# Kernel tuning notes

Hardware: AMD Instinct MI355X
Metric: run time of the kernel (lower is better)

Reference implementation:

```python
import jax, jax.numpy as jnp
import numpy as np

N_NODES = 100000
N_EDGES = 1600000
IN_CH = 128
TYPE_EMB = 32
OUT_CH = 128
N_REL = 8
N_BASES = 8
N_NTYPES = 8
FEAT = IN_CH + TYPE_EMB  # 160, RGCNConv input dim after concat


def setup_inputs() -> dict:
    key = jax.random.key(0)
    ks = jax.random.split(key, 9)
    x = jax.random.normal(ks[0], (N_NODES, IN_CH), dtype=jnp.float32)
    node_type_ids = jax.random.randint(ks[1], (N_NODES,), 0, N_NTYPES)
    edge_index = jax.random.randint(ks[2], (2, N_EDGES), 0, N_NODES)
    edge_type = jax.random.randint(ks[3], (N_EDGES,), 0, N_REL)
    emb_table = jax.random.normal(ks[4], (N_NTYPES, TYPE_EMB), dtype=jnp.float32)
    bases = jax.random.normal(ks[5], (N_BASES, FEAT, OUT_CH), dtype=jnp.float32) * (1.0 / np.sqrt(FEAT))
    comp = jax.random.normal(ks[6], (N_REL, N_BASES), dtype=jnp.float32) * (1.0 / np.sqrt(N_BASES))
    root_w = jax.random.normal(ks[7], (FEAT, OUT_CH), dtype=jnp.float32) * (1.0 / np.sqrt(FEAT))
    bias = jnp.zeros((OUT_CH,), dtype=jnp.float32)
    return {"x": x, "node_type_ids": node_type_ids, "edge_index": edge_index,
            "edge_type": edge_type, "emb_table": emb_table, "bases": bases,
            "comp": comp, "root_w": root_w, "bias": bias}


def reference(x, node_type_ids, edge_index, edge_type, emb_table, bases, comp, root_w, bias):
    N = x.shape[0]
    # node-type embedding lookup + concat
    h = jnp.concatenate([x, emb_table[node_type_ids]], axis=1)  # [N, FEAT]
    # basis decomposition: per-relation weights [R, FEAT, OUT]
    weight = jnp.einsum('rb,bio->rio', comp, bases)
    src, dst = edge_index[0], edge_index[1]
    h_src = h[src]  # [E, FEAT] -- dominant gather
    # root/self transform + bias
    out = h @ root_w + bias
    # PyG RGCNConv default aggr='mean': per-relation mean over incoming edges, summed across relations
    for r in range(weight.shape[0]):
        m = (edge_type == r).astype(h.dtype)  # [E]
        s = jax.ops.segment_sum(h_src * m[:, None], dst, num_segments=N)  # [N, FEAT]
        c = jax.ops.segment_sum(m, dst, num_segments=N)                    # [N]
        mean_r = s / jnp.maximum(c, 1.0)[:, None]
        out = out + mean_r @ weight[r]
    # dropout is identity in eval mode
    return jax.nn.relu(out)
```

## Files before the change

kernel.cpp:

```cpp
#include <hip/hip_runtime.h>

#define NN 100000
#define NE 1600000
#define INC 128
#define TE 32
#define OC 128
#define NR 8
#define NBASES 8
#define FT 160
#define KP 168
#define KW 160
#define TN 32
#define NBKT 3125
#define NCH 128
#define EPB 12500
#define CAP 896

typedef float f32x4 __attribute__((ext_vector_type(4)));
typedef float f32x2 __attribute__((ext_vector_type(2)));
typedef __bf16 bf16x8 __attribute__((ext_vector_type(8)));

__device__ __forceinline__ unsigned f2bf1(float f) {
    unsigned u = __float_as_uint(f);
    return (u + 0x7fffu + ((u >> 16) & 1u)) >> 16;
}

__device__ __forceinline__ float bflo(unsigned u) { return __uint_as_float(u << 16); }
__device__ __forceinline__ float bfhi(unsigned u) { return __uint_as_float(u & 0xFFFF0000u); }

__device__ __forceinline__ unsigned cvtpk(float a, float b) {
    unsigned r;
    asm("v_cvt_pk_bf16_f32 %0, %1, %2" : "=v"(r) : "v"(a), "v"(b));
    return r;
}

__device__ __forceinline__ int bscan_excl(int v, int* tmp) {
    int tid = threadIdx.x;
    tmp[tid] = v; __syncthreads();
#pragma unroll
    for (int d = 1; d < 256; d <<= 1) {
        int t = (tid >= d) ? tmp[tid - d] : 0;
        __syncthreads();
        tmp[tid] += t;
        __syncthreads();
    }
    return tmp[tid] - v;
}

__global__ __launch_bounds__(256) void k_prep(
    const float* __restrict__ x, const int* __restrict__ nt,
    const float* __restrict__ emb, const float* __restrict__ comp,
    const float* __restrict__ bases, const float* __restrict__ rootw,
    const int* __restrict__ ei,
    unsigned short* __restrict__ h, unsigned short* __restrict__ Wt,
    int* __restrict__ ghist, int* __restrict__ total) {
    __shared__ int hist[NBKT];
    int tid = threadIdx.x;
    int b = blockIdx.x;
    if (b < NCH) {
        for (int j = tid; j < NBKT; j += 256) hist[j] = 0;
        __syncthreads();
        int e0 = b * EPB;
#pragma unroll
        for (int k = 0; k < 49; k++) {
            int i = k * 256 + tid;
            if (i < EPB) atomicAdd(&hist[ei[NE + e0 + i] >> 5], 1);
        }
        __syncthreads();
        int* g = ghist + (size_t)b * NBKT;
        for (int j = tid; j < NBKT; j += 256) {
            int v = hist[j];
            g[j] = v;
            if (v) atomicAdd(&total[j], v);
        }
        return;
    }
    int idx = (b - NCH) * 256 + tid;
    if (idx < 9 * 128 * KW) {
        int ridx = idx / (128 * KW);
        int rem  = idx % (128 * KW);
        int o = rem / KW;
        int k = rem % KW;
        float v;
        if (ridx < NR) {
            v = 0.f;
#pragma unroll
            for (int bb = 0; bb < NBASES; bb++)
                v += comp[ridx * NBASES + bb] * bases[(bb * FT + k) * OC + o];
        } else {
            v = rootw[k * OC + o];
        }
        Wt[idx] = (unsigned short)f2bf1(v);
    }
    if (idx < NN * 16) {
        int n = idx / 16, c = idx % 16;
        const float* p = x + (size_t)n * INC + c * 8;
        f32x4 v0 = *(const f32x4*)p, v1 = *(const f32x4*)(p + 4);
        uint4 o;
        o.x = f2bf1(v0.x) | (f2bf1(v0.y) << 16);
        o.y = f2bf1(v0.z) | (f2bf1(v0.w) << 16);
        o.z = f2bf1(v1.x) | (f2bf1(v1.y) << 16);
        o.w = f2bf1(v1.z) | (f2bf1(v1.w) << 16);
        *(uint4*)(h + (size_t)n * INC + c * 8) = o;
    }
}

__global__ __launch_bounds__(256) void k_scanoff(const int* __restrict__ total,
                                                 int* __restrict__ ghist,
                                                 int* __restrict__ bstart) {
    __shared__ int tot[NBKT];
    __shared__ int tmp[256];
    int tid = threadIdx.x;
    for (int j = tid; j < NBKT; j += 256) tot[j] = total[j];
    __syncthreads();
    int i0 = tid * 13, s = 0;
    int loc[13];
#pragma unroll
    for (int i = 0; i < 13; i++) {
        int j = i0 + i;
        loc[i] = (j < NBKT) ? tot[j] : 0;
        s += loc[i];
    }
    int run = bscan_excl(s, tmp);
#pragma unroll
    for (int i = 0; i < 13; i++) {
        int j = i0 + i;
        if (j < NBKT) tot[j] = run;
        run += loc[i];
    }
    __syncthreads();
    if (blockIdx.x == 0) {
        for (int j = tid; j < NBKT; j += 256) bstart[j] = tot[j];
        if (tid == 0) bstart[NBKT] = NE;
    }
    int j = blockIdx.x * 256 + tid;
    if (j < NBKT) {
        int run2 = tot[j];
#pragma unroll 4
        for (int b = 0; b < NCH; b++) {
            int v = ghist[(size_t)b * NBKT + j];
            ghist[(size_t)b * NBKT + j] = run2;
            run2 += v;
        }
    }
}

__global__ __launch_bounds__(256) void k_scatter(const int* __restrict__ ei, const int* __restrict__ et,
                                                 const int* __restrict__ nt,
                                                 const int* __restrict__ ghist, unsigned* __restrict__ slots) {
    __shared__ int cur[NBKT];
    int tid = threadIdx.x, b = blockIdx.x;
    for (int j = tid; j < NBKT; j += 256) cur[j] = ghist[(size_t)b * NBKT + j];
    __syncthreads();
    int e0 = b * EPB;
#pragma unroll
    for (int kk = 0; kk < 52; kk += 4) {
        int sv[4], dv[4], rv[4], tv[4];
#pragma unroll
        for (int u = 0; u < 4; u++) {
            int i = (kk + u) * 256 + tid;
            int e = e0 + ((i < EPB) ? i : 0);
            sv[u] = ei[e]; dv[u] = ei[NE + e]; rv[u] = et[e];
            if (i >= EPB) dv[u] = -1;
        }
#pragma unroll
        for (int u = 0; u < 4; u++) tv[u] = nt[sv[u]];
#pragma unroll
        for (int u = 0; u < 4; u++) {
            if (dv[u] >= 0) {
                int pos = atomicAdd(&cur[dv[u] >> 5], 1);
                slots[pos] = (unsigned)sv[u] | ((unsigned)rv[u] << 17)
                           | ((unsigned)(dv[u] & 31) << 20) | ((unsigned)tv[u] << 25);
            }
        }
    }
}

__global__ __launch_bounds__(256, 6) void k_mega(
    const unsigned short* __restrict__ h, const int* __restrict__ nt,
    const float* __restrict__ emb, const float* __restrict__ bias,
    const unsigned short* __restrict__ Wt, const int* __restrict__ bstart,
    const unsigned* __restrict__ slots, float* __restrict__ out) {
    __shared__ unsigned short featmem[2][TN * KP];
    __shared__ unsigned sl[CAP];
    __shared__ unsigned pkl[256];
    __shared__ float embf[256];

    const int tid = threadIdx.x;
    const int lane = tid & 63;
    const int wave = tid >> 6;
    const int j = blockIdx.x;
    const int n0 = j * TN;

    unsigned* sl_in = reinterpret_cast<unsigned*>(&featmem[0][0]);
    int* hist = reinterpret_cast<int*>(&featmem[0][0]) + CAP;
    int* tmp  = reinterpret_cast<int*>(&featmem[0][0]) + CAP + 256;

    int s0 = bstart[j];
    int m = bstart[j + 1] - s0; if (m > CAP) m = CAP;
    for (int i = tid; i < m; i += 256) sl_in[i] = slots[s0 + i];
    hist[tid] = 0;
    __syncthreads();
    for (int i = tid; i < m; i += 256) {
        unsigned v = sl_in[i];
        atomicAdd(&hist[((v >> 17) & 7u) * 32u + ((v >> 20) & 31u)], 1);
    }
    __syncthreads();
    int v0 = hist[tid];
    int ex = bscan_excl(v0, tmp);
    pkl[tid] = (unsigned)ex | ((unsigned)v0 << 16);
    hist[tid] = ex;
    __syncthreads();
    for (int i = tid; i < m; i += 256) {
        unsigned v = sl_in[i];
        int p = atomicAdd(&hist[((v >> 17) & 7u) * 32u + ((v >> 20) & 31u)], 1);
        sl[p] = (v & 0x1FFFFu) | (((v >> 25) & 7u) << 17);
    }
    __syncthreads();

    if (tid < 256) embf[tid] = emb[tid];
    for (int i = tid; i < TN * 20; i += 256) {
        int nl = i / 20, c = i % 20, n = n0 + nl;
        uint4 v;
        if (c < 16) {
            v = *reinterpret_cast<const uint4*>(h + (size_t)n * INC + c * 8);
        } else {
            int t = nt[n];
            const float* p = emb + t * TE + (c - 16) * 8;
            f32x4 a = *(const f32x4*)p, bq = *(const f32x4*)(p + 4);
            v.x = f2bf1(a.x) | (f2bf1(a.y) << 16);
            v.y = f2bf1(a.z) | (f2bf1(a.w) << 16);
            v.z = f2bf1(bq.x) | (f2bf1(bq.y) << 16);
            v.w = f2bf1(bq.z) | (f2bf1(bq.w) << 16);
        }
        *reinterpret_cast<uint4*>(&featmem[0][nl * KP + c * 8]) = v;
    }

    f32x4 acc[4];
#pragma unroll
    for (int t = 0; t < 4; t++) acc[t] = (f32x4){0.f, 0.f, 0.f, 0.f};

    auto mfma_pass = [&](int ridx, const unsigned short* fm) {
        const unsigned short* fA = fm + (lane & 15) * KP + ((lane >> 4) * 8);
        const unsigned short* gB = Wt + (size_t)ridx * 128 * KW
                                   + (wave * 32 + (lane & 15)) * KW + ((lane >> 4) * 8);
#pragma unroll
        for (int kc = 0; kc < 5; kc++) {
            bf16x8 a0 = *reinterpret_cast<const bf16x8*>(fA + 0 * 16 * KP + kc * 32);
            bf16x8 a1 = *reinterpret_cast<const bf16x8*>(fA + 1 * 16 * KP + kc * 32);
#pragma unroll
            for (int ct = 0; ct < 2; ct++) {
                bf16x8 b = *reinterpret_cast<const bf16x8*>(gB + ct * 16 * KW + kc * 32);
                acc[0 * 2 + ct] = __builtin_amdgcn_mfma_f32_16x16x32_bf16(a0, b, acc[0 * 2 + ct], 0, 0, 0);
                acc[1 * 2 + ct] = __builtin_amdgcn_mfma_f32_16x16x32_bf16(a1, b, acc[1 * 2 + ct], 0, 0, 0);
            }
        }
    };

    const int g = tid >> 4, l = tid & 15;
    const unsigned* hw = reinterpret_cast<const unsigned*>(h);

    auto agg_pass = [&](int r, unsigned short* fm) {
        int b0 = r * 32 + 2 * g;
        unsigned pk0 = pkl[b0], pk1 = pkl[b0 + 1];
        int sbeg = (int)(pk0 & 0xffffu);
        int e1 = (int)(pk1 & 0xffffu);
        int send = e1 + (int)(pk1 >> 16);
        f32x2 sa[5];
#pragma unroll
        for (int i = 0; i < 5; i++) sa[i] = (f32x2){0.f, 0.f};
        float run = 0.f;
        for (int e = sbeg; e < send; e += 4) {
            uint4 wv[4]; int tt[4];
#pragma unroll
            for (int u = 0; u < 4; u++) {
                int eu = e + u; if (eu >= send) eu = send - 1;
                unsigned v = sl[eu];
                wv[u] = *reinterpret_cast<const uint4*>(hw + (size_t)(v & 0x1FFFFu) * 64 + 4 * l);
                tt[u] = (int)((v >> 17) & 7u);
            }
#pragma unroll
            for (int u = 0; u < 4; u++) {
                if (e + u < send) {
                    sa[0] += (f32x2){bflo(wv[u].x), bfhi(wv[u].x)};
                    sa[1] += (f32x2){bflo(wv[u].y), bfhi(wv[u].y)};
                    sa[2] += (f32x2){bflo(wv[u].z), bfhi(wv[u].z)};
                    sa[3] += (f32x2){bflo(wv[u].w), bfhi(wv[u].w)};
                    sa[4] += *reinterpret_cast<const f32x2*>(&embf[tt[u] * 32 + 2 * l]);
                    run += 1.f;
                    int nx = e + u + 1;
                    if (nx == e1 || nx == send) {
                        int q = (e + u >= e1) ? 1 : 0;
                        float inv = __builtin_amdgcn_rcpf(run);
                        f32x2 m0 = sa[0] * inv, m1 = sa[1] * inv, m2 = sa[2] * inv,
                              m3 = sa[3] * inv, m4 = sa[4] * inv;
                        unsigned* fp = reinterpret_cast<unsigned*>(fm + (2 * g + q) * KP);
                        uint4 o;
                        o.x = cvtpk(m0.x, m0.y);
                        o.y = cvtpk(m1.x, m1.y);
                        o.z = cvtpk(m2.x, m2.y);
                        o.w = cvtpk(m3.x, m3.y);
                        *reinterpret_cast<uint4*>(fp + 4 * l) = o;
                        fp[64 + l] = cvtpk(m4.x, m4.y);
#pragma unroll
                        for (int i = 0; i < 5; i++) sa[i] = (f32x2){0.f, 0.f};
                        run = 0.f;
                    }
                }
            }
        }
#pragma unroll
        for (int q = 0; q < 2; q++) {
            if ((pkl[b0 + q] >> 16) == 0u) {
                unsigned* fp = reinterpret_cast<unsigned*>(fm + (2 * g + q) * KP);
                *reinterpret_cast<uint4*>(fp + 4 * l) = (uint4){0u, 0u, 0u, 0u};
                fp[64 + l] = 0u;
            }
        }
    };

    __syncthreads();
    int prev = 8;
    for (int r = 0; r < NR; r++) {
        agg_pass(r, &featmem[(r + 1) & 1][0]);
        mfma_pass(prev, &featmem[r & 1][0]);
        prev = r;
        __syncthreads();
    }
    mfma_pass(7, &featmem[0][0]);

    const int rq = lane >> 4;
#pragma unroll
    for (int ct = 0; ct < 2; ct++) {
        int col = wave * 32 + ct * 16 + (lane & 15);
        float bv = bias[col];
#pragma unroll
        for (int rt = 0; rt < 2; rt++) {
#pragma unroll
            for (int i = 0; i < 4; i++) {
                int n = n0 + rt * 16 + rq * 4 + i;
                float v = acc[rt * 2 + ct][i] + bv;
                out[(size_t)n * OC + col] = v > 0.f ? v : 0.f;
            }
        }
    }
}

extern "C" void kernel_launch(void* const* d_in, const int* in_sizes, int n_in,
                              void* d_out, int out_size, void* d_ws, size_t ws_size,
                              hipStream_t stream) {
    const float* x     = (const float*)d_in[0];
    const int*   ntype = (const int*)d_in[1];
    const int*   ei    = (const int*)d_in[2];
    const int*   et    = (const int*)d_in[3];
    const float* emb   = (const float*)d_in[4];
    const float* bases = (const float*)d_in[5];
    const float* comp  = (const float*)d_in[6];
    const float* rootw = (const float*)d_in[7];
    const float* bias  = (const float*)d_in[8];
    float* out = (float*)d_out;

    char* ws = (char*)d_ws;
    unsigned short* Wt     = (unsigned short*)(ws);
    unsigned short* h      = (unsigned short*)(ws + 368640);
    int*            ghist  = (int*)(ws + 25968640);
    int*            total  = (int*)(ws + 27568640);
    int*            bstart = (int*)(ws + 27581184);
    unsigned*       slots  = (unsigned*)(ws + 27593728);

    hipMemsetAsync(total, 0, NBKT * sizeof(int), stream);
    k_prep   <<<NCH + 6250, 256, 0, stream>>>(x, ntype, emb, comp, bases, rootw, ei, h, Wt, ghist, total);
    k_scanoff<<<13,   256, 0, stream>>>(total, ghist, bstart);
    k_scatter<<<NCH,  256, 0, stream>>>(ei, et, ntype, ghist, slots);
    k_mega   <<<NBKT, 256, 0, stream>>>(h, ntype, emb, bias, Wt, bstart, slots, out);
}
```

Measured before the change: 376.3 us.

## Fold type embedding into weights via one-hot type fractions

Precomputes emb@W for each node type into the weight matrix rows 128-135, so the type-embedding part of each aggregated feature becomes a one-hot count fraction instead of a 32-wide embedding sum. This removes the shared-memory embedding reads and per-edge embedding accumulation in the aggregation loop, and the self-features use a one-hot type vector. The edge loop is also unrolled to 8 outstanding gathers. Folding the embedding before the bf16 rounding changes where rounding happens, and the prep kernel gains a small serial inner loop.

```diff
diff --git a/kernel.cpp b/kernel.cpp
--- a/kernel.cpp
+++ b/kernel.cpp
@@ -81,14 +81,29 @@
         int rem  = idx % (128 * KW);
         int o = rem / KW;
         int k = rem % KW;
-        float v;
-        if (ridx < NR) {
-            v = 0.f;
-#pragma unroll
-            for (int bb = 0; bb < NBASES; bb++)
-                v += comp[ridx * NBASES + bb] * bases[(bb * FT + k) * OC + o];
-        } else {
-            v = rootw[k * OC + o];
+        float v = 0.f;
+        if (k < 128) {
+            if (ridx < NR) {
+#pragma unroll
+                for (int bb = 0; bb < NBASES; bb++)
+                    v += comp[ridx * NBASES + bb] * bases[(bb * FT + k) * OC + o];
+            } else {
+                v = rootw[k * OC + o];
+            }
+        } else if (k < 136) {
+            int t = k - 128;
+            if (ridx < NR) {
+#pragma unroll
+                for (int bb = 0; bb < NBASES; bb++) {
+                    float cb = comp[ridx * NBASES + bb], s2 = 0.f;
+                    for (int k2 = 0; k2 < TE; k2++)
+                        s2 += emb[t * TE + k2] * bases[(bb * FT + 128 + k2) * OC + o];
+                    v += cb * s2;
+                }
+            } else {
+                for (int k2 = 0; k2 < TE; k2++)
+                    v += emb[t * TE + k2] * rootw[(128 + k2) * OC + o];
+            }
         }
         Wt[idx] = (unsigned short)f2bf1(v);
     }
@@ -178,13 +193,12 @@
 
 __global__ __launch_bounds__(256, 6) void k_mega(
     const unsigned short* __restrict__ h, const int* __restrict__ nt,
-    const float* __restrict__ emb, const float* __restrict__ bias,
+    const float* __restrict__ bias,
     const unsigned short* __restrict__ Wt, const int* __restrict__ bstart,
     const unsigned* __restrict__ slots, float* __restrict__ out) {
     __shared__ unsigned short featmem[2][TN * KP];
     __shared__ unsigned sl[CAP];
     __shared__ unsigned pkl[256];
-    __shared__ float embf[256];
 
     const int tid = threadIdx.x;
     const int lane = tid & 63;
@@ -218,20 +232,19 @@
     }
     __syncthreads();
 
-    if (tid < 256) embf[tid] = emb[tid];
     for (int i = tid; i < TN * 20; i += 256) {
         int nl = i / 20, c = i % 20, n = n0 + nl;
         uint4 v;
         if (c < 16) {
             v = *reinterpret_cast<const uint4*>(h + (size_t)n * INC + c * 8);
+        } else if (c == 16) {
+            int t = nt[n];
+            v.x = (t == 0 ? 0x3F80u : 0u) | (t == 1 ? 0x3F800000u : 0u);
+            v.y = (t == 2 ? 0x3F80u : 0u) | (t == 3 ? 0x3F800000u : 0u);
+            v.z = (t == 4 ? 0x3F80u : 0u) | (t == 5 ? 0x3F800000u : 0u);
+            v.w = (t == 6 ? 0x3F80u : 0u) | (t == 7 ? 0x3F800000u : 0u);
         } else {
-            int t = nt[n];
-            const float* p = emb + t * TE + (c - 16) * 8;
-            f32x4 a = *(const f32x4*)p, bq = *(const f32x4*)(p + 4);
-            v.x = f2bf1(a.x) | (f2bf1(a.y) << 16);
-            v.y = f2bf1(a.z) | (f2bf1(a.w) << 16);
-            v.z = f2bf1(bq.x) | (f2bf1(bq.y) << 16);
-            v.w = f2bf1(bq.z) | (f2bf1(bq.w) << 16);
+            v = (uint4){0u, 0u, 0u, 0u};
         }
         *reinterpret_cast<uint4*>(&featmem[0][nl * KP + c * 8]) = v;
     }
@@ -266,34 +279,37 @@
         int sbeg = (int)(pk0 & 0xffffu);
         int e1 = (int)(pk1 & 0xffffu);
         int send = e1 + (int)(pk1 >> 16);
-        f32x2 sa[5];
-#pragma unroll
-        for (int i = 0; i < 5; i++) sa[i] = (f32x2){0.f, 0.f};
+        f32x2 sa[4];
+#pragma unroll
+        for (int i = 0; i < 4; i++) sa[i] = (f32x2){0.f, 0.f};
+        f32x2 cnt2 = (f32x2){0.f, 0.f};
         float run = 0.f;
-        for (int e = sbeg; e < send; e += 4) {
-            uint4 wv[4]; int tt[4];
-#pragma unroll
-            for (int u = 0; u < 4; u++) {
+        for (int e = sbeg; e < send; e += 8) {
+            uint4 wv[8]; unsigned tpk = 0;
+#pragma unroll
+            for (int u = 0; u < 8; u++) {
                 int eu = e + u; if (eu >= send) eu = send - 1;
                 unsigned v = sl[eu];
                 wv[u] = *reinterpret_cast<const uint4*>(hw + (size_t)(v & 0x1FFFFu) * 64 + 4 * l);
-                tt[u] = (int)((v >> 17) & 7u);
-            }
-#pragma unroll
-            for (int u = 0; u < 4; u++) {
+                tpk |= ((v >> 17) & 7u) << (3 * u);
+            }
+#pragma unroll
+            for (int u = 0; u < 8; u++) {
                 if (e + u < send) {
                     sa[0] += (f32x2){bflo(wv[u].x), bfhi(wv[u].x)};
                     sa[1] += (f32x2){bflo(wv[u].y), bfhi(wv[u].y)};
                     sa[2] += (f32x2){bflo(wv[u].z), bfhi(wv[u].z)};
                     sa[3] += (f32x2){bflo(wv[u].w), bfhi(wv[u].w)};
-                    sa[4] += *reinterpret_cast<const f32x2*>(&embf[tt[u] * 32 + 2 * l]);
+                    int tt = (int)((tpk >> (3 * u)) & 7u);
+                    cnt2.x += (tt == 2 * l)     ? 1.f : 0.f;
+                    cnt2.y += (tt == 2 * l + 1) ? 1.f : 0.f;
                     run += 1.f;
                     int nx = e + u + 1;
                     if (nx == e1 || nx == send) {
                         int q = (e + u >= e1) ? 1 : 0;
                         float inv = __builtin_amdgcn_rcpf(run);
                         f32x2 m0 = sa[0] * inv, m1 = sa[1] * inv, m2 = sa[2] * inv,
-                              m3 = sa[3] * inv, m4 = sa[4] * inv;
+                              m3 = sa[3] * inv, fr = cnt2 * inv;
                         unsigned* fp = reinterpret_cast<unsigned*>(fm + (2 * g + q) * KP);
                         uint4 o;
                         o.x = cvtpk(m0.x, m0.y);
@@ -301,9 +317,10 @@
                         o.z = cvtpk(m2.x, m2.y);
                         o.w = cvtpk(m3.x, m3.y);
                         *reinterpret_cast<uint4*>(fp + 4 * l) = o;
-                        fp[64 + l] = cvtpk(m4.x, m4.y);
-#pragma unroll
-                        for (int i = 0; i < 5; i++) sa[i] = (f32x2){0.f, 0.f};
+                        fp[64 + l] = cvtpk(fr.x, fr.y);
+#pragma unroll
+                        for (int i = 0; i < 4; i++) sa[i] = (f32x2){0.f, 0.f};
+                        cnt2 = (f32x2){0.f, 0.f};
                         run = 0.f;
                     }
                 }
@@ -372,5 +389,5 @@
     k_prep   <<<NCH + 6250, 256, 0, stream>>>(x, ntype, emb, comp, bases, rootw, ei, h, Wt, ghist, total);
     k_scanoff<<<13,   256, 0, stream>>>(total, ghist, bstart);
     k_scatter<<<NCH,  256, 0, stream>>>(ei, et, ntype, ghist, slots);
-    k_mega   <<<NBKT, 256, 0, stream>>>(h, ntype, emb, bias, Wt, bstart, slots, out);
-}
+    k_mega   <<<NBKT, 256, 0, stream>>>(h, ntype, bias, Wt, bstart, slots, out);
+}
```

Result: slower. 514.5 us (+36.7%).
